# Kernel tuning notes

Measured on AMD Instinct MI355X. Metric: run time of the kernel, lower is better.

Reference implementation:

```python
import jax, jax.numpy as jnp
import numpy as np

RADIUS = 6
KERNEL = 2 * RADIUS + 1  # 13
TEMPERATURE = 0.07
EPS = 1e-12  # F.normalize eps


def setup_inputs() -> dict:
    key = jax.random.key(0)
    k1, k2 = jax.random.split(key)
    B, C, H, W = 4, 256, 128, 128
    f_a = jax.random.normal(k1, (B, C, H, W), dtype=jnp.float32)
    f_b = jax.random.normal(k2, (B, C, H, W), dtype=jnp.float32)
    return {"f_a": f_a, "f_b": f_b}


def _l2_normalize(x):
    # matches F.normalize(x, dim=1): x / max(||x||_2, eps)
    n = jnp.sqrt(jnp.sum(x * x, axis=1, keepdims=True))
    return x / jnp.maximum(n, EPS)


def reference(f_a, f_b):
    a = _l2_normalize(f_a)
    b = _l2_normalize(f_b)
    b_pad = jnp.pad(b, ((0, 0), (0, 0), (RADIUS, RADIUS), (RADIUS, RADIUS)))

    # offsets in the same (row-major ky, kx) order as F.unfold
    ky, kx = jnp.meshgrid(jnp.arange(KERNEL), jnp.arange(KERNEL), indexing="ij")
    offsets = jnp.stack([ky.ravel(), kx.ravel()], axis=-1)  # [K^2, 2]

    shape = f_a.shape  # (B, C, H, W)

    def step(carry, off):
        shifted = jax.lax.dynamic_slice(b_pad, (0, 0, off[0], off[1]), shape)
        c = jnp.einsum("bchw,bchw->bhw", a, shifted)
        return carry, c

    _, corr = jax.lax.scan(step, None, offsets)  # [K^2, B, H, W]
    corr = jnp.transpose(corr, (1, 0, 2, 3)) / TEMPERATURE  # [B, K^2, H, W]
    return corr
```

## Files before the change

kernel.cpp:

```cpp
#include <hip/hip_runtime.h>
#include <stdint.h>


typedef _Float16 half8 __attribute__((ext_vector_type(8)));
typedef float floatx4 __attribute__((ext_vector_type(4)));

#define B_ 4
#define C_ 256
#define H_ 128
#define W_ 128
#define K2_ 169
#define INV_T 14.285714285714286f
#define KGS (H_ * W_ * 32)
#define HW_ (H_ * W_)
#define P_OFF 40108032

static __device__ __forceinline__ void gload16(const void* g, void* l) {
  __builtin_amdgcn_global_load_lds((const __attribute__((address_space(1))) void*)g,
                                   (__attribute__((address_space(3))) void*)l, 16, 0, 0);
}

__global__ __launch_bounds__(256, 8) void norm_kernel(const float* __restrict__ fa,
                                                      const float* __restrict__ fb,
                                                      float* __restrict__ P) {
  const int bid = blockIdx.x;
  const int rg = bid & 15, cs = (bid >> 4) & 7, bb = (bid >> 7) & 3, tens = bid >> 9;
  const float* __restrict__ src = tens ? fb : fa;
  const int t = threadIdx.x;
  const float* gs = src + ((size_t)bb * C_ + cs * 32) * HW_ + rg * 1024 + t * 4;
  floatx4 acc = {0.f, 0.f, 0.f, 0.f};
  #pragma unroll
  for (int cc = 0; cc < 32; ++cc) {
    const floatx4 v = *(const floatx4*)(gs + (size_t)cc * HW_);
    acc += v * v;
  }
  *(floatx4*)(P + ((((size_t)tens * 4 + bb) * 8 + cs) * HW_) + rg * 1024 + t * 4) = acc;
}

__global__ __launch_bounds__(256, 6) void nt2_kernel(const float* __restrict__ fa,
                                                     const float* __restrict__ fb,
                                                     const float* __restrict__ P,
                                                     _Float16* __restrict__ an,
                                                     _Float16* __restrict__ bn) {
  const int bid = blockIdx.x;
  const int rg = bid & 63, kg = (bid >> 6) & 7, bb = (bid >> 9) & 3, tens = bid >> 11;
  const float* __restrict__ src = tens ? fb : fa;
  _Float16* __restrict__ dst = tens ? bn : an;
  const int t = threadIdx.x;
  const int w = t >> 6, l = t & 63, pxg = l >> 2, ccg = l & 3;
  const int pxq = rg * 256 + w * 64 + pxg * 4;

  const float* Pb = P + (((size_t)tens * 4 + bb) * 8) * HW_ + pxq;
  floatx4 s = {0.f, 0.f, 0.f, 0.f};
  #pragma unroll
  for (int cs = 0; cs < 8; ++cs) s += *(const floatx4*)(Pb + (size_t)cs * HW_);
  const float sc = tens ? 1.0f : INV_T;
  float inv[4];
  #pragma unroll
  for (int j = 0; j < 4; ++j) inv[j] = sc / fmaxf(sqrtf(s[j]), 1e-12f);

  const float* gs = src + ((size_t)bb * C_ + kg * 32 + ccg * 8) * HW_ + pxq;
  floatx4 v[8];
  #pragma unroll
  for (int cc = 0; cc < 8; ++cc) v[cc] = *(const floatx4*)(gs + (size_t)cc * HW_);

  _Float16* db = dst + ((size_t)bb * 8 + kg) * (size_t)HW_ * 32;
  #pragma unroll
  for (int j = 0; j < 4; ++j) {
    half8 h;
    #pragma unroll
    for (int cc = 0; cc < 8; ++cc) h[cc] = (_Float16)(v[cc][j] * inv[j]);
    *(half8*)(db + (size_t)(pxq + j) * 32 + ccg * 8) = h;
  }
}

union SmemU { _Float16 stage[2][16384]; float ostage[K2_ * 2 * 17]; };

__global__ __launch_bounds__(512, 4) void corr_kernel(const _Float16* __restrict__ an,
                                                      const _Float16* __restrict__ bn,
                                                      float* __restrict__ out) {
  __shared__ SmemU u;
  const int bid = blockIdx.x;
  const int xcd = bid & 7, l = bid >> 3;
  const int bb = l >> 5, hseg = (l >> 3) & 3, wt = l & 7;
  const int hg = xcd * 4 + hseg;
  const int h0 = hg * 4, w0 = wt * 16;
  const int t = threadIdx.x;
  const int lane = t & 63, wv = t >> 6;
  const int ml = lane & 15, q = lane >> 4;
  const int ntile = wv & 1, jjg = wv >> 1;

  const _Float16* ptr[4];
  unsigned flags = 0u;
  #pragma unroll
  for (int j = 0; j < 4; ++j) {
    const int job = j * 512 + t;
    if (job < 1792) {
      const int row = job / 112, rem = job - row * 112;
      const int col = rem >> 2, qt = rem & 3;
      const int rim = h0 - 6 + row, cim = w0 - 6 + col;
      const bool ok = ((unsigned)rim < (unsigned)H_) && ((unsigned)cim < (unsigned)W_);
      ptr[j] = bn + (((size_t)bb * 8 * H_ + (ok ? rim : 0)) * W_ + (ok ? cim : 0)) * 32 + qt * 8;
      if (ok) flags |= 1u << j;
    } else {
      const int aj = job - 1792;
      const int px = aj >> 2, qt = aj & 3;
      const int r = px >> 4, m = px & 15;
      ptr[j] = an + (((size_t)bb * 8 * H_ + h0 + r) * W_ + w0 + m) * 32 + qt * 8;
      flags |= 1u << j;
    }
  }

  const uint4 z4 = make_uint4(0u, 0u, 0u, 0u);
  #pragma unroll
  for (int j = 0; j < 4; ++j) {
    *(uint4*)((char*)u.stage[0] + (j * 512 + t) * 16) = z4;
    *(uint4*)((char*)u.stage[1] + (j * 512 + t) * 16) = z4;
  }
  __syncthreads();

  #pragma unroll
  for (int j = 0; j < 4; ++j) {
    if (flags & (1u << j))
      gload16(ptr[j], (char*)u.stage[0] + (j * 512 + wv * 64) * 16);
    ptr[j] += KGS;
  }

  floatx4 acc[4][4] = {};

  for (int kg = 0; kg < 8; ++kg) {
    __syncthreads();
    if (kg < 7) {
      char* nb = (char*)u.stage[(kg + 1) & 1];
      #pragma unroll
      for (int j = 0; j < 4; ++j) {
        if (flags & (1u << j))
          gload16(ptr[j], nb + (j * 512 + wv * 64) * 16);
        ptr[j] += KGS;
      }
    }
    const _Float16* sb = u.stage[kg & 1];

    half8 A[4];
    #pragma unroll
    for (int r = 0; r < 4; ++r)
      A[r] = *(const half8*)(sb + 14336 + (r * 16 + ml) * 32 + q * 8);

    #pragma unroll
    for (int uu = 0; uu < 4; ++uu) {
      const int jj = jjg + 4 * uu;
      const half8 Bf = *(const half8*)(sb + jj * 896 + (ntile * 16 + ml) * 32 + q * 8);
      #pragma unroll
      for (int r = 0; r < 4; ++r) {
        if ((uu == 0 && r > jjg) || (uu == 3 && r < jjg)) continue;
        acc[uu][r] = __builtin_amdgcn_mfma_f32_16x16x32_f16(A[r], Bf, acc[uu][r], 0, 0, 0);
      }
    }
  }

  #pragma unroll
  for (int r2 = 0; r2 < 2; ++r2) {
    if (r2) __syncthreads();
    #pragma unroll
    for (int uu = 0; uu < 4; ++uu) {
      const int jj = jjg + 4 * uu;
      const int col = ntile * 16 + ml;
      #pragma unroll
      for (int rr = 2 * r2; rr < 2 * r2 + 2; ++rr) {
        if ((uu == 0 && rr > jjg) || (uu == 3 && rr < jjg)) continue;
        const int dy6 = jj - rr;
        #pragma unroll
        for (int p = 0; p < 4; ++p) {
          const int ip = q * 4 + p;
          const int dx6 = col - ip;
          if (dx6 >= 0 && dx6 <= 12)
            u.ostage[((dy6 * 13 + dx6) * 2 + (rr & 1)) * 17 + ip] = acc[uu][rr][p];
        }
      }
    }
    __syncthreads();
    for (int s = t; s < K2_ * 32; s += 512) {
      const int k = s >> 5, r1 = (s >> 4) & 1, ip = s & 15;
      out[(((size_t)bb * K2_ + k) * H_ + h0 + 2 * r2 + r1) * W_ + w0 + ip] =
          u.ostage[(k * 2 + r1) * 17 + ip];
    }
  }
}

extern "C" void kernel_launch(void* const* d_in, const int* in_sizes, int n_in,
                              void* d_out, int out_size, void* d_ws, size_t ws_size,
                              hipStream_t stream) {
  const float* fa = (const float*)d_in[0];
  const float* fb = (const float*)d_in[1];
  float* out = (float*)d_out;
  float* P = (float*)((char*)d_out + P_OFF);
  _Float16* an = (_Float16*)d_ws;
  _Float16* bn = an + (size_t)B_ * H_ * W_ * C_;
  norm_kernel<<<1024, 256, 0, stream>>>(fa, fb, P);
  nt2_kernel<<<4096, 256, 0, stream>>>(fa, fb, P, an, bn);
  corr_kernel<<<1024, 512, 0, stream>>>(an, bn, out);
}
```

Before: 219.6 us.

## Fuse normalization into correlation kernel, reading fp32 inputs directly per tile

Replaces the three-kernel pipeline (norm partial sums, normalize-and-convert to fp16 workspace, correlation) with a single kernel. Each block loads raw fp32 features for its haloed tile, converts them to fp16 in LDS, and accumulates squared norms along the way. The normalization is applied afterwards as per-pixel scales on the dot products. This removes the intermediate fp16 workspace round-trip and two kernel launches. The cost is that halo pixels are re-read redundantly in fp32 by neighbouring blocks (about 28x7 vs 16x4), the loads are strided per channel with scalar accesses instead of async global_load_lds, and un-normalized fp16 values may lose precision.

```diff
diff --git a/kernel.cpp b/kernel.cpp
--- a/kernel.cpp
+++ b/kernel.cpp
@@ -11,75 +11,16 @@
 #define W_ 128
 #define K2_ 169
 #define INV_T 14.285714285714286f
-#define KGS (H_ * W_ * 32)
 #define HW_ (H_ * W_)
-#define P_OFF 40108032
-
-static __device__ __forceinline__ void gload16(const void* g, void* l) {
-  __builtin_amdgcn_global_load_lds((const __attribute__((address_space(1))) void*)g,
-                                   (__attribute__((address_space(3))) void*)l, 16, 0, 0);
-}
-
-__global__ __launch_bounds__(256, 8) void norm_kernel(const float* __restrict__ fa,
-                                                      const float* __restrict__ fb,
-                                                      float* __restrict__ P) {
-  const int bid = blockIdx.x;
-  const int rg = bid & 15, cs = (bid >> 4) & 7, bb = (bid >> 7) & 3, tens = bid >> 9;
-  const float* __restrict__ src = tens ? fb : fa;
-  const int t = threadIdx.x;
-  const float* gs = src + ((size_t)bb * C_ + cs * 32) * HW_ + rg * 1024 + t * 4;
-  floatx4 acc = {0.f, 0.f, 0.f, 0.f};
-  #pragma unroll
-  for (int cc = 0; cc < 32; ++cc) {
-    const floatx4 v = *(const floatx4*)(gs + (size_t)cc * HW_);
-    acc += v * v;
-  }
-  *(floatx4*)(P + ((((size_t)tens * 4 + bb) * 8 + cs) * HW_) + rg * 1024 + t * 4) = acc;
-}
-
-__global__ __launch_bounds__(256, 6) void nt2_kernel(const float* __restrict__ fa,
-                                                     const float* __restrict__ fb,
-                                                     const float* __restrict__ P,
-                                                     _Float16* __restrict__ an,
-                                                     _Float16* __restrict__ bn) {
-  const int bid = blockIdx.x;
-  const int rg = bid & 63, kg = (bid >> 6) & 7, bb = (bid >> 9) & 3, tens = bid >> 11;
-  const float* __restrict__ src = tens ? fb : fa;
-  _Float16* __restrict__ dst = tens ? bn : an;
-  const int t = threadIdx.x;
-  const int w = t >> 6, l = t & 63, pxg = l >> 2, ccg = l & 3;
-  const int pxq = rg * 256 + w * 64 + pxg * 4;
-
-  const float* Pb = P + (((size_t)tens * 4 + bb) * 8) * HW_ + pxq;
-  floatx4 s = {0.f, 0.f, 0.f, 0.f};
-  #pragma unroll
-  for (int cs = 0; cs < 8; ++cs) s += *(const floatx4*)(Pb + (size_t)cs * HW_);
-  const float sc = tens ? 1.0f : INV_T;
-  float inv[4];
-  #pragma unroll
-  for (int j = 0; j < 4; ++j) inv[j] = sc / fmaxf(sqrtf(s[j]), 1e-12f);
-
-  const float* gs = src + ((size_t)bb * C_ + kg * 32 + ccg * 8) * HW_ + pxq;
-  floatx4 v[8];
-  #pragma unroll
-  for (int cc = 0; cc < 8; ++cc) v[cc] = *(const floatx4*)(gs + (size_t)cc * HW_);
-
-  _Float16* db = dst + ((size_t)bb * 8 + kg) * (size_t)HW_ * 32;
-  #pragma unroll
-  for (int j = 0; j < 4; ++j) {
-    half8 h;
-    #pragma unroll
-    for (int cc = 0; cc < 8; ++cc) h[cc] = (_Float16)(v[cc][j] * inv[j]);
-    *(half8*)(db + (size_t)(pxq + j) * 32 + ccg * 8) = h;
-  }
-}
 
 union SmemU { _Float16 stage[2][16384]; float ostage[K2_ * 2 * 17]; };
 
-__global__ __launch_bounds__(512, 4) void corr_kernel(const _Float16* __restrict__ an,
-                                                      const _Float16* __restrict__ bn,
-                                                      float* __restrict__ out) {
+__global__ __launch_bounds__(512, 4) void corr_fused(const float* __restrict__ fa,
+                                                     const float* __restrict__ fb,
+                                                     float* __restrict__ out) {
   __shared__ SmemU u;
+  __shared__ float inv_b[448];
+  __shared__ float inv_a[64];
   const int bid = blockIdx.x;
   const int xcd = bid & 7, l = bid >> 3;
   const int bb = l >> 5, hseg = (l >> 3) & 3, wt = l & 7;
@@ -90,55 +31,49 @@
   const int ml = lane & 15, q = lane >> 4;
   const int ntile = wv & 1, jjg = wv >> 1;
 
-  const _Float16* ptr[4];
-  unsigned flags = 0u;
-  #pragma unroll
-  for (int j = 0; j < 4; ++j) {
-    const int job = j * 512 + t;
-    if (job < 1792) {
-      const int row = job / 112, rem = job - row * 112;
-      const int col = rem >> 2, qt = rem & 3;
-      const int rim = h0 - 6 + row, cim = w0 - 6 + col;
-      const bool ok = ((unsigned)rim < (unsigned)H_) && ((unsigned)cim < (unsigned)W_);
-      ptr[j] = bn + (((size_t)bb * 8 * H_ + (ok ? rim : 0)) * W_ + (ok ? cim : 0)) * 32 + qt * 8;
-      if (ok) flags |= 1u << j;
-    } else {
-      const int aj = job - 1792;
-      const int px = aj >> 2, qt = aj & 3;
-      const int r = px >> 4, m = px & 15;
-      ptr[j] = an + (((size_t)bb * 8 * H_ + h0 + r) * W_ + w0 + m) * 32 + qt * 8;
-      flags |= 1u << j;
-    }
+  bool ok;
+  const float* gp;
+  int pxo;
+  if (t < 448) {
+    const int row = t / 28, col = t - row * 28;
+    const int rim = h0 - 6 + row, cim = w0 - 6 + col;
+    ok = ((unsigned)rim < (unsigned)H_) && ((unsigned)cim < (unsigned)W_);
+    gp = fb + (size_t)bb * C_ * HW_ + (ok ? (rim * W_ + cim) : 0);
+    pxo = t * 32;
+  } else {
+    const int px = t - 448;
+    const int r = px >> 4, m = px & 15;
+    ok = true;
+    gp = fa + (size_t)bb * C_ * HW_ + (h0 + r) * W_ + (w0 + m);
+    pxo = 14336 + px * 32;
   }
 
-  const uint4 z4 = make_uint4(0u, 0u, 0u, 0u);
-  #pragma unroll
-  for (int j = 0; j < 4; ++j) {
-    *(uint4*)((char*)u.stage[0] + (j * 512 + t) * 16) = z4;
-    *(uint4*)((char*)u.stage[1] + (j * 512 + t) * 16) = z4;
-  }
-  __syncthreads();
+  float ss = 0.f;
+  float v[32];
 
   #pragma unroll
-  for (int j = 0; j < 4; ++j) {
-    if (flags & (1u << j))
-      gload16(ptr[j], (char*)u.stage[0] + (j * 512 + wv * 64) * 16);
-    ptr[j] += KGS;
+  for (int cc = 0; cc < 32; ++cc) v[cc] = ok ? gp[(size_t)cc * HW_] : 0.f;
+  gp += (size_t)32 * HW_;
+  {
+    _Float16* wb = u.stage[0] + pxo;
+    #pragma unroll
+    for (int qq = 0; qq < 4; ++qq) {
+      half8 hh;
+      #pragma unroll
+      for (int j = 0; j < 8; ++j) { const float x = v[qq * 8 + j]; ss += x * x; hh[j] = (_Float16)x; }
+      *(half8*)(wb + qq * 8) = hh;
+    }
   }
 
   floatx4 acc[4][4] = {};
 
   for (int kg = 0; kg < 8; ++kg) {
+    if (kg < 7) {
+      #pragma unroll
+      for (int cc = 0; cc < 32; ++cc) v[cc] = ok ? gp[(size_t)cc * HW_] : 0.f;
+      gp += (size_t)32 * HW_;
+    }
     __syncthreads();
-    if (kg < 7) {
-      char* nb = (char*)u.stage[(kg + 1) & 1];
-      #pragma unroll
-      for (int j = 0; j < 4; ++j) {
-        if (flags & (1u << j))
-          gload16(ptr[j], nb + (j * 512 + wv * 64) * 16);
-        ptr[j] += KGS;
-      }
-    }
     const _Float16* sb = u.stage[kg & 1];
 
     half8 A[4];
@@ -156,7 +91,22 @@
         acc[uu][r] = __builtin_amdgcn_mfma_f32_16x16x32_f16(A[r], Bf, acc[uu][r], 0, 0, 0);
       }
     }
+
+    if (kg < 7) {
+      _Float16* wb = u.stage[(kg + 1) & 1] + pxo;
+      #pragma unroll
+      for (int qq = 0; qq < 4; ++qq) {
+        half8 hh;
+        #pragma unroll
+        for (int j = 0; j < 8; ++j) { const float x = v[qq * 8 + j]; ss += x * x; hh[j] = (_Float16)x; }
+        *(half8*)(wb + qq * 8) = hh;
+      }
+    }
   }
+
+  if (t < 448) inv_b[t] = 1.0f / fmaxf(sqrtf(ss), 1e-12f);
+  else         inv_a[t - 448] = INV_T / fmaxf(sqrtf(ss), 1e-12f);
+  __syncthreads();
 
   #pragma unroll
   for (int r2 = 0; r2 < 2; ++r2) {
@@ -165,6 +115,7 @@
     for (int uu = 0; uu < 4; ++uu) {
       const int jj = jjg + 4 * uu;
       const int col = ntile * 16 + ml;
+      const float sbv = (col < 28) ? inv_b[jj * 28 + col] : 0.f;
       #pragma unroll
       for (int rr = 2 * r2; rr < 2 * r2 + 2; ++rr) {
         if ((uu == 0 && rr > jjg) || (uu == 3 && rr < jjg)) continue;
@@ -174,7 +125,8 @@
           const int ip = q * 4 + p;
           const int dx6 = col - ip;
           if (dx6 >= 0 && dx6 <= 12)
-            u.ostage[((dy6 * 13 + dx6) * 2 + (rr & 1)) * 17 + ip] = acc[uu][rr][p];
+            u.ostage[((dy6 * 13 + dx6) * 2 + (rr & 1)) * 17 + ip] =
+                acc[uu][rr][p] * sbv * inv_a[rr * 16 + ip];
         }
       }
     }
@@ -193,10 +145,6 @@
   const float* fa = (const float*)d_in[0];
   const float* fb = (const float*)d_in[1];
   float* out = (float*)d_out;
-  float* P = (float*)((char*)d_out + P_OFF);
-  _Float16* an = (_Float16*)d_ws;
-  _Float16* bn = an + (size_t)B_ * H_ * W_ * C_;
-  norm_kernel<<<1024, 256, 0, stream>>>(fa, fb, P);
-  nt2_kernel<<<4096, 256, 0, stream>>>(fa, fb, P, an, bn);
-  corr_kernel<<<1024, 512, 0, stream>>>(an, bn, out);
+  (void)d_ws; (void)ws_size;
+  corr_fused<<<1024, 512, 0, stream>>>(fa, fb, out);
 }
```

Result: faster. 210.9 us (-4.0%).
